# Kernel optimization log

Hardware: AMD Instinct MI355X
Metric: run time of the kernel (lower is better)

The kernel has to match this reference:

```python
import jax, jax.numpy as jnp
import numpy as np

L, E, H, NH, S_MAX, V, NL = 3, 512, 64, 8, 512, 30522, 2  # layers, d_model, head_dim, heads, max_len, vocab, labels
LN_EPS = 1e-5


def _layer_norm(x, g, b):
    m = jnp.mean(x, axis=-1, keepdims=True)
    v = jnp.mean((x - m) ** 2, axis=-1, keepdims=True)
    return (x - m) * jax.lax.rsqrt(v + LN_EPS) * g + b


def setup_inputs() -> dict:
    key = jax.random.key(0)
    ks = jax.random.split(key, 20)
    B, S = 32, 512
    inp = {
        'input_ids': jax.random.randint(ks[0], (B, S), 0, V, dtype=jnp.int64 if jax.config.jax_enable_x64 else jnp.int32),
        'attention_mask': jnp.ones((B, S), dtype=jnp.int32),
        # embeddings (padding_idx=0 row zeroed, as in nn.Embedding(padding_idx=0))
        'emb': (0.02 * jax.random.normal(ks[1], (V, E), jnp.float32)).at[0].set(0.0),
        'pos_emb': 0.02 * jax.random.normal(ks[2], (S_MAX, E), jnp.float32),
        # per-layer stacked params, leading dim = L
        'in_proj_w': 0.02 * jax.random.normal(ks[3], (L, 3 * E, E), jnp.float32),
        'in_proj_b': jnp.zeros((L, 3 * E), jnp.float32),
        'out_proj_w': 0.02 * jax.random.normal(ks[4], (L, E, E), jnp.float32),
        'out_proj_b': jnp.zeros((L, E), jnp.float32),
        'ln1_g': jnp.ones((L, E), jnp.float32), 'ln1_b': jnp.zeros((L, E), jnp.float32),
        'ln2_g': jnp.ones((L, E), jnp.float32), 'ln2_b': jnp.zeros((L, E), jnp.float32),
        'ffn1_w': 0.02 * jax.random.normal(ks[5], (L, 4 * E, E), jnp.float32),
        'ffn1_b': jnp.zeros((L, 4 * E), jnp.float32),
        'ffn2_w': 0.02 * jax.random.normal(ks[6], (L, E, 4 * E), jnp.float32),
        'ffn2_b': jnp.zeros((L, E), jnp.float32),
        'cls_w': 0.02 * jax.random.normal(ks[7], (NL, E), jnp.float32),
        'cls_b': jnp.zeros((NL,), jnp.float32),
    }
    return inp


def reference(input_ids, attention_mask, emb, pos_emb, in_proj_w, in_proj_b,
              out_proj_w, out_proj_b, ln1_g, ln1_b, ln2_g, ln2_b,
              ffn1_w, ffn1_b, ffn2_w, ffn2_b, cls_w, cls_b):
    B, S = input_ids.shape
    x = emb[input_ids] + pos_emb[jnp.arange(S)][None, :, :]  # [B,S,E]
    # key_padding_mask: True where attention_mask == 0 -> -inf on key axis
    kpm_bias = jnp.where((attention_mask == 0)[:, None, None, :], -jnp.inf, 0.0)  # [B,1,1,S]
    scale = 1.0 / np.sqrt(H)
    attns = []
    for l in range(L):
        qkv = x @ in_proj_w[l].T + in_proj_b[l]          # [B,S,3E]
        q, k, v = jnp.split(qkv, 3, axis=-1)
        q = q.reshape(B, S, NH, H).transpose(0, 2, 1, 3)  # [B,NH,S,H]
        k = k.reshape(B, S, NH, H).transpose(0, 2, 1, 3)
        v = v.reshape(B, S, NH, H).transpose(0, 2, 1, 3)
        scores = jnp.einsum('bhqd,bhkd->bhqk', q, k) * scale + kpm_bias
        a = jax.nn.softmax(scores, axis=-1)               # materialized per-head weights [B,NH,S,S]
        o = jnp.einsum('bhqk,bhkd->bhqd', a, v).transpose(0, 2, 1, 3).reshape(B, S, E)
        o = o @ out_proj_w[l].T + out_proj_b[l]
        x = _layer_norm(x + o, ln1_g[l], ln1_b[l])
        f = jax.nn.gelu(x @ ffn1_w[l].T + ffn1_b[l], approximate=False)
        f = f @ ffn2_w[l].T + ffn2_b[l]
        x = _layer_norm(x + f, ln2_g[l], ln2_b[l])
        attns.append(a)
    logits = x[:, 0, :] @ cls_w.T + cls_b                 # CLS token head
    return logits, jnp.stack(attns)                       # ([B,NL], [L,B,NH,S,S])
```

## Files before the change

### kernel.cpp

```cpp
#include <hip/hip_runtime.h>
#include <hip/hip_bf16.h>


typedef __bf16 bf16_t;
typedef __bf16 bf16x4 __attribute__((ext_vector_type(4)));
typedef __bf16 bf16x8 __attribute__((ext_vector_type(8)));
typedef float  f32x4  __attribute__((ext_vector_type(4)));

__device__ __forceinline__ void gld16(const bf16_t* g, bf16_t* l) {
    __builtin_amdgcn_global_load_lds((const __attribute__((address_space(1))) void*)g,
                                     (__attribute__((address_space(3))) void*)l, 16, 0, 0);
}

__global__ __launch_bounds__(256) void cvt_bf16(
    const float* __restrict__ s, bf16_t* __restrict__ d)
{
    int g = blockIdx.x * 256 + threadIdx.x;
    float4 v = ((const float4*)s)[g];
    bf16x4 p;
    p[0] = (bf16_t)v.x; p[1] = (bf16_t)v.y; p[2] = (bf16_t)v.z; p[3] = (bf16_t)v.w;
    ((bf16x4*)d)[g] = p;
}

__global__ __launch_bounds__(256) void embed_kernel(
    const int* __restrict__ ids, const float* __restrict__ emb,
    const float* __restrict__ pos, float* __restrict__ x, bf16_t* __restrict__ xb)
{
    int g = blockIdx.x * 256 + threadIdx.x;
    int token = g >> 7, c4 = g & 127;
    int id = ids[token];
    float4 e = ((const float4*)emb)[(long long)id * 128 + c4];
    float4 p = ((const float4*)pos)[(long long)(token & 511) * 128 + c4];
    e.x += p.x; e.y += p.y; e.z += p.z; e.w += p.w;
    ((float4*)x)[g] = e;
    bf16x4 h;
    h[0] = (bf16_t)e.x; h[1] = (bf16_t)e.y; h[2] = (bf16_t)e.z; h[3] = (bf16_t)e.w;
    ((bf16x4*)xb)[g] = h;
}

template<int BN, int AF32, int GELU, int OBF>
__global__ __launch_bounds__(256) void gemm_m97(
    const void* __restrict__ Ap, const bf16_t* __restrict__ Bp,
    void* __restrict__ Cp, const float* __restrict__ bias,
    int lda, int ldb, int ldc, int K,
    long long sAb, long long sAh, long long sBb, long long sBh,
    long long sCb, long long sCh, float alpha)
{
    constexpr int WR = (BN == 128) ? 2 : 4;
    constexpr int WM = 128 / WR;
    constexpr int MI = WM / 16;

    __shared__ __align__(16) bf16_t As[128 * 64];
    __shared__ __align__(16) bf16_t Bs[BN * 64];

    const int m0 = blockIdx.x * 128, n0 = blockIdx.y * BN;
    const int z = blockIdx.z, zb = z >> 3, zh = z & 7;

    const bf16_t* A  = (const bf16_t*)Ap;
    const float*  Af = (const float*)Ap;
    if (AF32) Af += zb * sAb + zh * sAh + (long long)m0 * lda;
    else      A  += zb * sAb + zh * sAh + (long long)m0 * lda;
    const bf16_t* B = Bp + zb * sBb + zh * sBh + (long long)n0 * ldb;

    const int tid = threadIdx.x, wave = tid >> 6, lane = tid & 63;
    const int q = lane >> 4, r = lane & 15;
    const int wr = wave % WR, wc = wave / WR;

    f32x4 acc[MI][4];
#pragma unroll
    for (int i = 0; i < MI; i++)
#pragma unroll
        for (int j = 0; j < 4; j++) acc[i][j] = (f32x4){0.f, 0.f, 0.f, 0.f};

    for (int k0 = 0; k0 < K; k0 += 64) {
        if (AF32) {
#pragma unroll
            for (int it = 0; it < 8; it++) {
                int chunk = it * 256 + tid;
                int row = chunk >> 4, c4 = (chunk & 15) << 2;
                float4 v = *(const float4*)(Af + (long long)row * lda + k0 + c4);
                bf16x4 p;
                p[0] = (bf16_t)v.x; p[1] = (bf16_t)v.y; p[2] = (bf16_t)v.z; p[3] = (bf16_t)v.w;
                *(bf16x4*)(As + row * 64 + c4) = p;
            }
        } else {
#pragma unroll
            for (int it = 0; it < 4; it++) {
                int chunk = it * 256 + tid;
                int row = chunk >> 3, c8 = (chunk & 7) << 3;
                gld16(A + (long long)row * lda + k0 + c8,
                      As + (it * 256 + wave * 64) * 8);
            }
        }
#pragma unroll
        for (int it = 0; it < BN / 32; it++) {
            int chunk = it * 256 + tid;
            int row = chunk >> 3, c8 = (chunk & 7) << 3;
            gld16(B + (long long)row * ldb + k0 + c8,
                  Bs + (it * 256 + wave * 64) * 8);
        }
        __syncthreads();
#pragma unroll
        for (int kk = 0; kk < 64; kk += 32) {
            bf16x8 av[MI], bv[4];
#pragma unroll
            for (int mi = 0; mi < MI; mi++)
                av[mi] = *(const bf16x8*)(As + (wr * WM + mi * 16 + r) * 64 + kk + q * 8);
#pragma unroll
            for (int ni = 0; ni < 4; ni++)
                bv[ni] = *(const bf16x8*)(Bs + (wc * 64 + ni * 16 + r) * 64 + kk + q * 8);
#pragma unroll
            for (int mi = 0; mi < MI; mi++)
#pragma unroll
                for (int ni = 0; ni < 4; ni++)
                    acc[mi][ni] = __builtin_amdgcn_mfma_f32_16x16x32_bf16(
                        av[mi], bv[ni], acc[mi][ni], 0, 0, 0);
        }
        __syncthreads();
    }

    const long long cb = (long long)zb * sCb + (long long)zh * sCh;
#pragma unroll
    for (int ni = 0; ni < 4; ni++) {
        int col = n0 + wc * 64 + ni * 16 + r;
        float bvl = bias ? bias[col] : 0.f;
#pragma unroll
        for (int mi = 0; mi < MI; mi++) {
#pragma unroll
            for (int i = 0; i < 4; i++) {
                int row = m0 + wr * WM + mi * 16 + q * 4 + i;
                float v = acc[mi][ni][i] * alpha + bvl;
                if (GELU) v = 0.5f * v * (1.f + erff(v * 0.70710678118654752f));
                if (OBF) ((bf16_t*)Cp)[cb + (long long)row * ldc + col] = (bf16_t)v;
                else     ((float*)Cp)[cb + (long long)row * ldc + col] = v;
            }
        }
    }
}

__global__ __launch_bounds__(256) void attn_scores_softmax(
    const bf16_t* __restrict__ qkv, const int* __restrict__ amask,
    float* __restrict__ attn)
{
    __shared__ __align__(16) bf16_t Ks[512 * 64];
    __shared__ float bias_s[512];

    const int z = blockIdx.y, b = z >> 3, h = z & 7;
    const int q0 = blockIdx.x * 64;
    const int tid = threadIdx.x, wave = tid >> 6, lane = tid & 63;
    const int q = lane >> 4, r = lane & 15;

    const bf16_t* Kg = qkv + (long long)(b * 512) * 1536 + 512 + h * 64;
#pragma unroll
    for (int it = 0; it < 16; it++) {
        int chunk = it * 256 + tid;
        int row = chunk >> 3, c8 = (chunk & 7) << 3;
        gld16(Kg + (long long)row * 1536 + c8, Ks + (it * 256 + wave * 64) * 8);
    }
    {
        int i0 = tid * 2;
        bias_s[i0]     = (amask[b * 512 + i0]     == 0) ? -__builtin_inff() : 0.f;
        bias_s[i0 + 1] = (amask[b * 512 + i0 + 1] == 0) ? -__builtin_inff() : 0.f;
    }
    const bf16_t* Qg = qkv + (long long)(b * 512 + q0 + wave * 16 + r) * 1536 + h * 64;
    bf16x8 av0 = *(const bf16x8*)(Qg + q * 8);
    bf16x8 av1 = *(const bf16x8*)(Qg + 32 + q * 8);
    __syncthreads();

    f32x4 acc[32];
#pragma unroll
    for (int nf = 0; nf < 32; nf++) acc[nf] = (f32x4){0.f, 0.f, 0.f, 0.f};

#pragma unroll
    for (int nf = 0; nf < 32; nf++) {
        bf16x8 b0 = *(const bf16x8*)(Ks + (nf * 16 + r) * 64 + q * 8);
        bf16x8 b1 = *(const bf16x8*)(Ks + (nf * 16 + r) * 64 + 32 + q * 8);
        acc[nf] = __builtin_amdgcn_mfma_f32_16x16x32_bf16(av0, b0, acc[nf], 0, 0, 0);
        acc[nf] = __builtin_amdgcn_mfma_f32_16x16x32_bf16(av1, b1, acc[nf], 0, 0, 0);
    }

    float mx[4] = {-3.0e38f, -3.0e38f, -3.0e38f, -3.0e38f};
#pragma unroll
    for (int nf = 0; nf < 32; nf++) {
        float bl = bias_s[nf * 16 + r];
#pragma unroll
        for (int i = 0; i < 4; i++) {
            float s = acc[nf][i] * 0.125f + bl;
            acc[nf][i] = s;
            mx[i] = fmaxf(mx[i], s);
        }
    }
#pragma unroll
    for (int off = 8; off; off >>= 1)
#pragma unroll
        for (int i = 0; i < 4; i++) mx[i] = fmaxf(mx[i], __shfl_xor(mx[i], off));

    float sm[4] = {0.f, 0.f, 0.f, 0.f};
#pragma unroll
    for (int nf = 0; nf < 32; nf++)
#pragma unroll
        for (int i = 0; i < 4; i++) {
            float e = __expf(acc[nf][i] - mx[i]);
            acc[nf][i] = e;
            sm[i] += e;
        }
#pragma unroll
    for (int off = 8; off; off >>= 1)
#pragma unroll
        for (int i = 0; i < 4; i++) sm[i] += __shfl_xor(sm[i], off);

    float inv[4];
#pragma unroll
    for (int i = 0; i < 4; i++) inv[i] = 1.f / sm[i];

    float* out = attn + (long long)z * 262144 + (long long)(q0 + wave * 16) * 512;
#pragma unroll
    for (int nf = 0; nf < 32; nf++)
#pragma unroll
        for (int i = 0; i < 4; i++)
            out[(q * 4 + i) * 512 + nf * 16 + r] = acc[nf][i] * inv[i];
}

__global__ __launch_bounds__(256) void transpose_v(
    const bf16_t* __restrict__ qkv, bf16_t* __restrict__ Vt)
{
    int z = blockIdx.x, b = z >> 3, h = z & 7;
    int k0 = blockIdx.y * 64;
    __shared__ bf16_t t[64][72];
    const bf16_t* src = qkv + (long long)(b * 512 + k0) * 1536 + 1024 + h * 64;
    int tid = threadIdx.x;
#pragma unroll
    for (int it = 0; it < 2; it++) {
        int idx = tid + 256 * it;
        int i = idx >> 3, j8 = (idx & 7) << 3;
        bf16x8 v = *(const bf16x8*)(src + (long long)i * 1536 + j8);
#pragma unroll
        for (int j = 0; j < 8; j++) t[i][j8 + j] = v[j];
    }
    __syncthreads();
    bf16_t* dst = Vt + (long long)z * 32768 + k0;
#pragma unroll
    for (int it = 0; it < 2; it++) {
        int idx = tid + 256 * it;
        int d = idx >> 3, kx = (idx & 7) << 3;
        bf16x8 v;
#pragma unroll
        for (int j = 0; j < 8; j++) v[j] = t[kx + j][d];
        *(bf16x8*)(dst + (long long)d * 512 + kx) = v;
    }
}

__global__ __launch_bounds__(256) void add_ln(
    float* __restrict__ x, const float* __restrict__ rsd,
    const float* __restrict__ g, const float* __restrict__ bta,
    bf16_t* __restrict__ xb)
{
    long long row = (long long)blockIdx.x * 4 + (threadIdx.x >> 6);
    int lane = threadIdx.x & 63;
    float4* xr = (float4*)(x + row * 512);
    const float4* rr = (const float4*)(rsd + row * 512);
    float4 s0 = xr[lane], s1 = xr[lane + 64];
    float4 r0 = rr[lane], r1 = rr[lane + 64];
    s0.x += r0.x; s0.y += r0.y; s0.z += r0.z; s0.w += r0.w;
    s1.x += r1.x; s1.y += r1.y; s1.z += r1.z; s1.w += r1.w;
    float sum = s0.x + s0.y + s0.z + s0.w + s1.x + s1.y + s1.z + s1.w;
    float sq  = s0.x*s0.x + s0.y*s0.y + s0.z*s0.z + s0.w*s0.w
              + s1.x*s1.x + s1.y*s1.y + s1.z*s1.z + s1.w*s1.w;
#pragma unroll
    for (int o = 32; o; o >>= 1) { sum += __shfl_xor(sum, o); sq += __shfl_xor(sq, o); }
    float mean = sum * (1.f / 512.f);
    float var  = sq * (1.f / 512.f) - mean * mean;
    float rstd = rsqrtf(var + 1e-5f);
    const float4* g4 = (const float4*)g;
    const float4* b4 = (const float4*)bta;
    float4 gg = g4[lane], bb = b4[lane], o0;
    o0.x = (s0.x - mean) * rstd * gg.x + bb.x;
    o0.y = (s0.y - mean) * rstd * gg.y + bb.y;
    o0.z = (s0.z - mean) * rstd * gg.z + bb.z;
    o0.w = (s0.w - mean) * rstd * gg.w + bb.w;
    xr[lane] = o0;
    bf16x4 h0;
    h0[0] = (bf16_t)o0.x; h0[1] = (bf16_t)o0.y; h0[2] = (bf16_t)o0.z; h0[3] = (bf16_t)o0.w;
    *(bf16x4*)(xb + row * 512 + lane * 4) = h0;
    gg = g4[lane + 64]; bb = b4[lane + 64];
    float4 o1;
    o1.x = (s1.x - mean) * rstd * gg.x + bb.x;
    o1.y = (s1.y - mean) * rstd * gg.y + bb.y;
    o1.z = (s1.z - mean) * rstd * gg.z + bb.z;
    o1.w = (s1.w - mean) * rstd * gg.w + bb.w;
    xr[lane + 64] = o1;
    bf16x4 h1;
    h1[0] = (bf16_t)o1.x; h1[1] = (bf16_t)o1.y; h1[2] = (bf16_t)o1.z; h1[3] = (bf16_t)o1.w;
    *(bf16x4*)(xb + row * 512 + 256 + lane * 4) = h1;
}

__global__ void cls_head(const float* __restrict__ x, const float* __restrict__ w,
                         const float* __restrict__ cb, float* __restrict__ out)
{
    int b = blockIdx.x >> 1, c = blockIdx.x & 1;
    int lane = threadIdx.x;
    const float* xr = x + (long long)b * 512 * 512;
    const float* wr = w + c * 512;
    float s = 0.f;
#pragma unroll
    for (int i = 0; i < 8; i++) s += xr[lane + 64 * i] * wr[lane + 64 * i];
#pragma unroll
    for (int o = 32; o; o >>= 1) s += __shfl_xor(s, o);
    if (lane == 0) out[b * 2 + c] = s + cb[c];
}

extern "C" void kernel_launch(void* const* d_in, const int* in_sizes, int n_in,
                              void* d_out, int out_size, void* d_ws, size_t ws_size,
                              hipStream_t stream)
{
    const int*   ids   = (const int*)d_in[0];
    const int*   amask = (const int*)d_in[1];
    const float* emb   = (const float*)d_in[2];
    const float* pos   = (const float*)d_in[3];
    const float* in_w  = (const float*)d_in[4];
    const float* in_b  = (const float*)d_in[5];
    const float* out_w = (const float*)d_in[6];
    const float* out_b = (const float*)d_in[7];
    const float* ln1g  = (const float*)d_in[8];
    const float* ln1b  = (const float*)d_in[9];
    const float* ln2g  = (const float*)d_in[10];
    const float* ln2b  = (const float*)d_in[11];
    const float* f1w   = (const float*)d_in[12];
    const float* f1b   = (const float*)d_in[13];
    const float* f2w   = (const float*)d_in[14];
    const float* f2b   = (const float*)d_in[15];
    const float* clsw  = (const float*)d_in[16];
    const float* clsb  = (const float*)d_in[17];

    float* outp = (float*)d_out;
    float* ws = (float*)d_ws;
    float*  x    = ws;
    bf16_t* xb   = (bf16_t*)(ws + 8388608);
    float*  pg   = ws + 12582912;
    bf16_t* Ob   = (bf16_t*)(ws + 20971520);
    bf16_t* qkvb = (bf16_t*)(ws + 25165824);
    bf16_t* Vt   = (bf16_t*)(ws + 37748736);
    bf16_t* fb   = qkvb;
    bf16_t* wb   = (bf16_t*)(ws + 41943040);
    bf16_t* w_in  = wb;
    bf16_t* w_out = wb + 2359296;
    bf16_t* w_f1  = wb + 3145728;
    bf16_t* w_f2  = wb + 6291456;

    cvt_bf16<<<2304, 256, 0, stream>>>(in_w,  w_in);
    cvt_bf16<<< 768, 256, 0, stream>>>(out_w, w_out);
    cvt_bf16<<<3072, 256, 0, stream>>>(f1w,   w_f1);
    cvt_bf16<<<3072, 256, 0, stream>>>(f2w,   w_f2);

    embed_kernel<<<8192, 256, 0, stream>>>(ids, emb, pos, x, xb);

    for (int l = 0; l < 3; l++) {
        float* attnL = outp + 64 + (long long)l * 67108864;

        gemm_m97<128, 0, 0, 1><<<dim3(128, 12, 1), 256, 0, stream>>>(
            xb, w_in + (long long)l * 786432, qkvb, in_b + l * 1536,
            512, 512, 1536, 512, 0, 0, 0, 0, 0, 0, 1.f);

        transpose_v<<<dim3(256, 8), 256, 0, stream>>>(qkvb, Vt);

        attn_scores_softmax<<<dim3(8, 256), 256, 0, stream>>>(qkvb, amask, attnL);

        gemm_m97<64, 1, 0, 1><<<dim3(4, 1, 256), 256, 0, stream>>>(
            attnL, Vt, Ob, nullptr,
            512, 512, 512, 512,
            2097152, 262144, 262144, 32768, 262144, 64, 1.f);

        gemm_m97<128, 0, 0, 0><<<dim3(128, 4, 1), 256, 0, stream>>>(
            Ob, w_out + (long long)l * 262144, pg, out_b + l * 512,
            512, 512, 512, 512, 0, 0, 0, 0, 0, 0, 1.f);

        add_ln<<<4096, 256, 0, stream>>>(x, pg, ln1g + l * 512, ln1b + l * 512, xb);

        gemm_m97<128, 0, 1, 1><<<dim3(128, 16, 1), 256, 0, stream>>>(
            xb, w_f1 + (long long)l * 1048576, fb, f1b + l * 2048,
            512, 512, 2048, 512, 0, 0, 0, 0, 0, 0, 1.f);

        gemm_m97<128, 0, 0, 0><<<dim3(128, 4, 1), 256, 0, stream>>>(
            fb, w_f2 + (long long)l * 1048576, pg, f2b + l * 512,
            2048, 2048, 512, 2048, 0, 0, 0, 0, 0, 0, 1.f);

        add_ln<<<4096, 256, 0, stream>>>(x, pg, ln2g + l * 512, ln2b + l * 512, xb);
    }

    cls_head<<<64, 64, 0, stream>>>(x, clsw, clsb, outp);
}
```

Measured before the change: 2.069 ms.

## Fuse attention P@V into scores-softmax kernel, drop fp32 attention reread

The separate batched GEMM that re-read the fp32 attention probabilities from global memory to multiply by V is removed. The softmax kernel now also loads the transposed V head slice into shared memory, writes normalized probabilities as bf16 into the reused K buffer, and runs the P@V MFMA itself, writing the head output directly. This avoids a large fp32 global reread per layer and one launch. In exchange, shared memory per block roughly doubles (about 130KB), which lowers occupancy. The GEMM template is simplified to the remaining single-batch shape.

```diff
diff --git a/kernel.cpp b/kernel.cpp
--- a/kernel.cpp
+++ b/kernel.cpp
@@ -38,79 +38,49 @@
     ((bf16x4*)xb)[g] = h;
 }
 
-template<int BN, int AF32, int GELU, int OBF>
+template<int GELU, int OBF>
 __global__ __launch_bounds__(256) void gemm_m97(
-    const void* __restrict__ Ap, const bf16_t* __restrict__ Bp,
+    const bf16_t* __restrict__ A, const bf16_t* __restrict__ B,
     void* __restrict__ Cp, const float* __restrict__ bias,
-    int lda, int ldb, int ldc, int K,
-    long long sAb, long long sAh, long long sBb, long long sBh,
-    long long sCb, long long sCh, float alpha)
-{
-    constexpr int WR = (BN == 128) ? 2 : 4;
-    constexpr int WM = 128 / WR;
-    constexpr int MI = WM / 16;
-
+    int lda, int ldb, int ldc, int K, float alpha)
+{
     __shared__ __align__(16) bf16_t As[128 * 64];
-    __shared__ __align__(16) bf16_t Bs[BN * 64];
-
-    const int m0 = blockIdx.x * 128, n0 = blockIdx.y * BN;
-    const int z = blockIdx.z, zb = z >> 3, zh = z & 7;
-
-    const bf16_t* A  = (const bf16_t*)Ap;
-    const float*  Af = (const float*)Ap;
-    if (AF32) Af += zb * sAb + zh * sAh + (long long)m0 * lda;
-    else      A  += zb * sAb + zh * sAh + (long long)m0 * lda;
-    const bf16_t* B = Bp + zb * sBb + zh * sBh + (long long)n0 * ldb;
+    __shared__ __align__(16) bf16_t Bs[128 * 64];
+
+    const int m0 = blockIdx.x * 128, n0 = blockIdx.y * 128;
+    A += (long long)m0 * lda;
+    B += (long long)n0 * ldb;
 
     const int tid = threadIdx.x, wave = tid >> 6, lane = tid & 63;
     const int q = lane >> 4, r = lane & 15;
-    const int wr = wave % WR, wc = wave / WR;
-
-    f32x4 acc[MI][4];
-#pragma unroll
-    for (int i = 0; i < MI; i++)
+    const int wr = wave & 1, wc = wave >> 1;
+
+    f32x4 acc[4][4];
+#pragma unroll
+    for (int i = 0; i < 4; i++)
 #pragma unroll
         for (int j = 0; j < 4; j++) acc[i][j] = (f32x4){0.f, 0.f, 0.f, 0.f};
 
     for (int k0 = 0; k0 < K; k0 += 64) {
-        if (AF32) {
-#pragma unroll
-            for (int it = 0; it < 8; it++) {
-                int chunk = it * 256 + tid;
-                int row = chunk >> 4, c4 = (chunk & 15) << 2;
-                float4 v = *(const float4*)(Af + (long long)row * lda + k0 + c4);
-                bf16x4 p;
-                p[0] = (bf16_t)v.x; p[1] = (bf16_t)v.y; p[2] = (bf16_t)v.z; p[3] = (bf16_t)v.w;
-                *(bf16x4*)(As + row * 64 + c4) = p;
-            }
-        } else {
-#pragma unroll
-            for (int it = 0; it < 4; it++) {
-                int chunk = it * 256 + tid;
-                int row = chunk >> 3, c8 = (chunk & 7) << 3;
-                gld16(A + (long long)row * lda + k0 + c8,
-                      As + (it * 256 + wave * 64) * 8);
-            }
-        }
-#pragma unroll
-        for (int it = 0; it < BN / 32; it++) {
+#pragma unroll
+        for (int it = 0; it < 4; it++) {
             int chunk = it * 256 + tid;
             int row = chunk >> 3, c8 = (chunk & 7) << 3;
-            gld16(B + (long long)row * ldb + k0 + c8,
-                  Bs + (it * 256 + wave * 64) * 8);
+            gld16(A + (long long)row * lda + k0 + c8, As + (it * 256 + wave * 64) * 8);
+            gld16(B + (long long)row * ldb + k0 + c8, Bs + (it * 256 + wave * 64) * 8);
         }
         __syncthreads();
 #pragma unroll
         for (int kk = 0; kk < 64; kk += 32) {
-            bf16x8 av[MI], bv[4];
-#pragma unroll
-            for (int mi = 0; mi < MI; mi++)
-                av[mi] = *(const bf16x8*)(As + (wr * WM + mi * 16 + r) * 64 + kk + q * 8);
+            bf16x8 av[4], bv[4];
+#pragma unroll
+            for (int mi = 0; mi < 4; mi++)
+                av[mi] = *(const bf16x8*)(As + (wr * 64 + mi * 16 + r) * 64 + kk + q * 8);
 #pragma unroll
             for (int ni = 0; ni < 4; ni++)
                 bv[ni] = *(const bf16x8*)(Bs + (wc * 64 + ni * 16 + r) * 64 + kk + q * 8);
 #pragma unroll
-            for (int mi = 0; mi < MI; mi++)
+            for (int mi = 0; mi < 4; mi++)
 #pragma unroll
                 for (int ni = 0; ni < 4; ni++)
                     acc[mi][ni] = __builtin_amdgcn_mfma_f32_16x16x32_bf16(
@@ -119,30 +89,31 @@
         __syncthreads();
     }
 
-    const long long cb = (long long)zb * sCb + (long long)zh * sCh;
 #pragma unroll
     for (int ni = 0; ni < 4; ni++) {
         int col = n0 + wc * 64 + ni * 16 + r;
         float bvl = bias ? bias[col] : 0.f;
 #pragma unroll
-        for (int mi = 0; mi < MI; mi++) {
+        for (int mi = 0; mi < 4; mi++) {
 #pragma unroll
             for (int i = 0; i < 4; i++) {
-                int row = m0 + wr * WM + mi * 16 + q * 4 + i;
+                int row = m0 + wr * 64 + mi * 16 + q * 4 + i;
                 float v = acc[mi][ni][i] * alpha + bvl;
                 if (GELU) v = 0.5f * v * (1.f + erff(v * 0.70710678118654752f));
-                if (OBF) ((bf16_t*)Cp)[cb + (long long)row * ldc + col] = (bf16_t)v;
-                else     ((float*)Cp)[cb + (long long)row * ldc + col] = v;
+                if (OBF) ((bf16_t*)Cp)[(long long)row * ldc + col] = (bf16_t)v;
+                else     ((float*)Cp)[(long long)row * ldc + col] = v;
             }
         }
     }
 }
 
-__global__ __launch_bounds__(256) void attn_scores_softmax(
-    const bf16_t* __restrict__ qkv, const int* __restrict__ amask,
-    float* __restrict__ attn)
+__global__ __launch_bounds__(256) void attn_fused(
+    const bf16_t* __restrict__ qkv, const bf16_t* __restrict__ Vt,
+    const int* __restrict__ amask, float* __restrict__ attn,
+    bf16_t* __restrict__ Ob)
 {
     __shared__ __align__(16) bf16_t Ks[512 * 64];
+    __shared__ __align__(16) bf16_t Vs[64 * 512];
     __shared__ float bias_s[512];
 
     const int z = blockIdx.y, b = z >> 3, h = z & 7;
@@ -157,6 +128,13 @@
         int row = chunk >> 3, c8 = (chunk & 7) << 3;
         gld16(Kg + (long long)row * 1536 + c8, Ks + (it * 256 + wave * 64) * 8);
     }
+    const bf16_t* Vg = Vt + (long long)z * 32768;
+#pragma unroll
+    for (int it = 0; it < 16; it++) {
+        int chunk = it * 256 + tid;
+        int row = chunk >> 6, c8 = (chunk & 63) << 3;
+        gld16(Vg + (long long)row * 512 + c8, Vs + (it * 256 + wave * 64) * 8);
+    }
     {
         int i0 = tid * 2;
         bias_s[i0]     = (amask[b * 512 + i0]     == 0) ? -__builtin_inff() : 0.f;
@@ -170,7 +148,6 @@
     f32x4 acc[32];
 #pragma unroll
     for (int nf = 0; nf < 32; nf++) acc[nf] = (f32x4){0.f, 0.f, 0.f, 0.f};
-
 #pragma unroll
     for (int nf = 0; nf < 32; nf++) {
         bf16x8 b0 = *(const bf16x8*)(Ks + (nf * 16 + r) * 64 + q * 8);
@@ -208,17 +185,45 @@
     for (int off = 8; off; off >>= 1)
 #pragma unroll
         for (int i = 0; i < 4; i++) sm[i] += __shfl_xor(sm[i], off);
-
     float inv[4];
 #pragma unroll
     for (int i = 0; i < 4; i++) inv[i] = 1.f / sm[i];
 
+    __syncthreads();
+
+    bf16_t* P = Ks;
     float* out = attn + (long long)z * 262144 + (long long)(q0 + wave * 16) * 512;
 #pragma unroll
-    for (int nf = 0; nf < 32; nf++)
+    for (int nf = 0; nf < 32; nf++) {
+#pragma unroll
+        for (int i = 0; i < 4; i++) {
+            float pv = acc[nf][i] * inv[i];
+            int rr = q * 4 + i, cc = nf * 16 + r;
+            out[(long long)rr * 512 + cc] = pv;
+            P[(wave * 16 + rr) * 512 + cc] = (bf16_t)pv;
+        }
+    }
+    __syncthreads();
+
+    f32x4 oacc[4];
+#pragma unroll
+    for (int ni = 0; ni < 4; ni++) oacc[ni] = (f32x4){0.f, 0.f, 0.f, 0.f};
+#pragma unroll
+    for (int ks = 0; ks < 16; ks++) {
+        bf16x8 pa = *(const bf16x8*)(P + (wave * 16 + r) * 512 + ks * 32 + q * 8);
+#pragma unroll
+        for (int ni = 0; ni < 4; ni++) {
+            bf16x8 vb = *(const bf16x8*)(Vs + (ni * 16 + r) * 512 + ks * 32 + q * 8);
+            oacc[ni] = __builtin_amdgcn_mfma_f32_16x16x32_bf16(pa, vb, oacc[ni], 0, 0, 0);
+        }
+    }
+
+    bf16_t* ob = Ob + (long long)(b * 512 + q0 + wave * 16) * 512 + h * 64;
+#pragma unroll
+    for (int ni = 0; ni < 4; ni++)
 #pragma unroll
         for (int i = 0; i < 4; i++)
-            out[(q * 4 + i) * 512 + nf * 16 + r] = acc[nf][i] * inv[i];
+            ob[(long long)(q * 4 + i) * 512 + ni * 16 + r] = (bf16_t)oacc[ni][i];
 }
 
 __global__ __launch_bounds__(256) void transpose_v(
@@ -357,32 +362,27 @@
     for (int l = 0; l < 3; l++) {
         float* attnL = outp + 64 + (long long)l * 67108864;
 
-        gemm_m97<128, 0, 0, 1><<<dim3(128, 12, 1), 256, 0, stream>>>(
+        gemm_m97<0, 1><<<dim3(128, 12, 1), 256, 0, stream>>>(
             xb, w_in + (long long)l * 786432, qkvb, in_b + l * 1536,
-            512, 512, 1536, 512, 0, 0, 0, 0, 0, 0, 1.f);
+            512, 512, 1536, 512, 1.f);
 
         transpose_v<<<dim3(256, 8), 256, 0, stream>>>(qkvb, Vt);
 
-        attn_scores_softmax<<<dim3(8, 256), 256, 0, stream>>>(qkvb, amask, attnL);
-
-        gemm_m97<64, 1, 0, 1><<<dim3(4, 1, 256), 256, 0, stream>>>(
-            attnL, Vt, Ob, nullptr,
-            512, 512, 512, 512,
-            2097152, 262144, 262144, 32768, 262144, 64, 1.f);
-
-        gemm_m97<128, 0, 0, 0><<<dim3(128, 4, 1), 256, 0, stream>>>(
+        attn_fused<<<dim3(8, 256), 256, 0, stream>>>(qkvb, Vt, amask, attnL, Ob);
+
+        gemm_m97<0, 0><<<dim3(128, 4, 1), 256, 0, stream>>>(
             Ob, w_out + (long long)l * 262144, pg, out_b + l * 512,
-            512, 512, 512, 512, 0, 0, 0, 0, 0, 0, 1.f);
+            512, 512, 512, 512, 1.f);
 
         add_ln<<<4096, 256, 0, stream>>>(x, pg, ln1g + l * 512, ln1b + l * 512, xb);
 
-        gemm_m97<128, 0, 1, 1><<<dim3(128, 16, 1), 256, 0, stream>>>(
+        gemm_m97<1, 1><<<dim3(128, 16, 1), 256, 0, stream>>>(
             xb, w_f1 + (long long)l * 1048576, fb, f1b + l * 2048,
-            512, 512, 2048, 512, 0, 0, 0, 0, 0, 0, 1.f);
-
-        gemm_m97<128, 0, 0, 0><<<dim3(128, 4, 1), 256, 0, stream>>>(
+            512, 512, 2048, 512, 1.f);
+
+        gemm_m97<0, 0><<<dim3(128, 4, 1), 256, 0, stream>>>(
             fb, w_f2 + (long long)l * 1048576, pg, f2b + l * 512,
-            2048, 2048, 512, 2048, 0, 0, 0, 0, 0, 0, 1.f);
+            2048, 2048, 512, 2048, 1.f);
 
         add_ln<<<4096, 256, 0, stream>>>(x, pg, ln2g + l * 512, ln2b + l * 512, xb);
     }
```

Result: faster. 1.991 ms (-3.8%).
